# Performance work log

Hardware: AMD Instinct MI355X
Metric: run time of the kernel (lower is better)

## Reference

```python
import jax, jax.numpy as jnp
import numpy as np

B, LT, LS, D, H, F = 4, 1024, 1024, 1024, 16, 4096
HD = D // H
EPS = 1e-6


def rms_norm(x, g):
    return x / jnp.sqrt(jnp.mean(x * x, axis=-1, keepdims=True) + EPS) * g


def mha(q_in, kv_in, wq, wk, wv, wo, bias):
    # q_in: [B,Lq,D], kv_in: [B,Lk,D], bias broadcastable to [B,H,Lq,Lk]
    b, lq, _ = q_in.shape
    lk = kv_in.shape[1]
    q = (q_in @ wq).reshape(b, lq, H, HD).transpose(0, 2, 1, 3)
    k = (kv_in @ wk).reshape(b, lk, H, HD).transpose(0, 2, 1, 3)
    v = (kv_in @ wv).reshape(b, lk, H, HD).transpose(0, 2, 1, 3)
    s = jnp.einsum('bhqd,bhkd->bhqk', q, k) / np.sqrt(HD).astype(np.float32) + bias
    o = jnp.einsum('bhqk,bhkd->bhqd', jax.nn.softmax(s, axis=-1), v)
    o = o.transpose(0, 2, 1, 3).reshape(b, lq, D) @ wo
    return o, k, v


def setup_inputs() -> dict:
    key = jax.random.key(0)
    ks = jax.random.split(key, 16)
    f = lambda k, sh, s: jax.random.normal(k, sh, jnp.float32) * s
    wscale = 1.0 / float(np.sqrt(D))
    causal = jnp.where(jnp.triu(jnp.ones((LT, LT), bool), 1), jnp.float32(-1e9), jnp.float32(0.0))
    return {
        'x': f(ks[0], (B, LT, D), 1.0),
        'memory': f(ks[1], (B, LS, D), 1.0),
        'position_embedding': f(ks[2], (1, H, LT, LS), 0.02),
        'causal_mask': causal,
        'gamma_sa': jnp.ones((D,), jnp.float32),
        'wq_s': f(ks[3], (D, D), wscale), 'wk_s': f(ks[4], (D, D), wscale),
        'wv_s': f(ks[5], (D, D), wscale), 'wo_s': f(ks[6], (D, D), wscale),
        'gamma_ca': jnp.ones((D,), jnp.float32),
        'wq_c': f(ks[7], (D, D), wscale), 'wk_c': f(ks[8], (D, D), wscale),
        'wv_c': f(ks[9], (D, D), wscale), 'wo_c': f(ks[10], (D, D), wscale),
        'gamma_m': jnp.ones((D,), jnp.float32),
        'w1': f(ks[11], (D, F), wscale), 'w2': f(ks[12], (F, D), 1.0 / float(np.sqrt(F))),
    }


def reference(x, memory, position_embedding, causal_mask,
              gamma_sa, wq_s, wk_s, wv_s, wo_s,
              gamma_ca, wq_c, wk_c, wv_c, wo_c,
              gamma_m, w1, w2):
    # self-attention block (pre-RMSNorm, causal mask, residual)
    h = rms_norm(x, gamma_sa)
    a, k_s, v_s = mha(h, h, wq_s, wk_s, wv_s, wo_s, causal_mask[None, None, :, :])
    attn_x = a + x
    # cross-attention block (position-embedding bias on scores, residual)
    h2 = rms_norm(attn_x, gamma_ca)
    c, k_c, v_c = mha(h2, memory, wq_c, wk_c, wv_c, wo_c, position_embedding)
    cross_x = c + attn_x
    # FFN block
    h3 = rms_norm(cross_x, gamma_m)
    mlp_x = jax.nn.relu(h3 @ w1) @ w2 + cross_x
    return mlp_x, (k_s, v_s), (k_c, v_c)
```

## Files before the change

### kernel.cpp

```cpp
#include <hip/hip_runtime.h>
#include <stdint.h>
#include <stddef.h>

typedef __bf16 bf16_t;
typedef __attribute__((ext_vector_type(8))) __bf16 bf16x8;
typedef __attribute__((ext_vector_type(4))) float f32x4;

#define LT 1024
#define LS 1024
#define DM 1024
#define NH 16
#define HD 64
#define FF 4096
#define BB 4

__device__ __forceinline__ void gld_lds16(const bf16_t* g, bf16_t* l) {
    __builtin_amdgcn_global_load_lds(
        (const __attribute__((address_space(1))) void*)g,
        (__attribute__((address_space(3))) void*)l, 16, 0, 0);
}

__global__ __launch_bounds__(256) void transpose_f2bf(
    const float* __restrict__ in, bf16_t* __restrict__ out, int R, int C)
{
    __shared__ float tile[32][33];
    int bx = blockIdx.x * 32;
    int by = blockIdx.y * 32;
    int tx = threadIdx.x, ty = threadIdx.y;
#pragma unroll
    for (int j = 0; j < 4; j++)
        tile[ty + j * 8][tx] = in[(size_t)(by + ty + j * 8) * C + bx + tx];
    __syncthreads();
#pragma unroll
    for (int j = 0; j < 4; j++)
        out[(size_t)(bx + ty + j * 8) * R + by + tx] = (bf16_t)tile[tx][ty + j * 8];
}

__global__ __launch_bounds__(256) void transpose_bf(
    const bf16_t* __restrict__ in, bf16_t* __restrict__ out)
{
    __shared__ bf16_t tile[32][33];
    int bh = blockIdx.z;
    int r0 = blockIdx.x * 32;
    int c0 = blockIdx.y * 32;
    const bf16_t* ib = in + (size_t)bh * LT * HD;
    bf16_t* ob = out + (size_t)bh * HD * LT;
    int tx = threadIdx.x, ty = threadIdx.y;
#pragma unroll
    for (int j = 0; j < 4; j++)
        tile[ty + j * 8][tx] = ib[(size_t)(r0 + ty + j * 8) * HD + c0 + tx];
    __syncthreads();
#pragma unroll
    for (int j = 0; j < 4; j++)
        ob[(size_t)(c0 + ty + j * 8) * LT + r0 + tx] = tile[tx][ty + j * 8];
}

__global__ __launch_bounds__(256) void f2bf_kernel(
    const float* __restrict__ in, bf16_t* __restrict__ out, size_t n)
{
    size_t i = ((size_t)blockIdx.x * 256 + threadIdx.x) * 4;
    if (i + 3 < n) {
        float4 v = *(const float4*)&in[i];
        out[i + 0] = (bf16_t)v.x;
        out[i + 1] = (bf16_t)v.y;
        out[i + 2] = (bf16_t)v.z;
        out[i + 3] = (bf16_t)v.w;
    }
}

__global__ __launch_bounds__(256) void reduce2_res(
    const float* __restrict__ p, const float* __restrict__ res,
    float* __restrict__ out)
{
    const size_t MN = (size_t)BB * LT * DM;
    size_t i = ((size_t)blockIdx.x * 256 + threadIdx.x) * 4;
    float4 a = *(const float4*)&p[i];
    float4 b = *(const float4*)&p[i + MN];
    float4 r = *(const float4*)&res[i];
    float4 o;
    o.x = a.x + b.x + r.x; o.y = a.y + b.y + r.y;
    o.z = a.z + b.z + r.z; o.w = a.w + b.w + r.w;
    *(float4*)&out[i] = o;
}

__global__ __launch_bounds__(256) void rmsnorm_kernel(
    const float* __restrict__ x, const float* __restrict__ g,
    bf16_t* __restrict__ out)
{
    __shared__ float red[4];
    int row = blockIdx.x;
    int t = threadIdx.x;
    int lane = t & 63, w = t >> 6;
    const float* xr = x + (size_t)row * DM;
    float4 v = *(const float4*)&xr[t * 4];
    float ss = v.x * v.x + v.y * v.y + v.z * v.z + v.w * v.w;
#pragma unroll
    for (int off = 32; off > 0; off >>= 1) ss += __shfl_down(ss, off, 64);
    if (lane == 0) red[w] = ss;
    __syncthreads();
    float tot = red[0] + red[1] + red[2] + red[3];
    float inv = rsqrtf(tot * (1.0f / DM) + 1e-6f);
    float4 gv = *(const float4*)&g[t * 4];
    bf16_t* o = out + (size_t)row * DM + t * 4;
    o[0] = (bf16_t)(v.x * inv * gv.x);
    o[1] = (bf16_t)(v.y * inv * gv.y);
    o[2] = (bf16_t)(v.z * inv * gv.z);
    o[3] = (bf16_t)(v.w * inv * gv.w);
}

#define GEMM_BODY(Aptr, Btptr, Kstride, kBeg, kEnd)                              \
    for (int k0 = (kBeg); k0 < (kEnd); k0 += 64) {                               \
        __syncthreads();                                                         \
        _Pragma("unroll")                                                        \
        for (int i = 0; i < 4; i++) {                                            \
            int p = i * 256 + t;                                                 \
            int row = p >> 3;                                                    \
            int g = (p & 7) ^ (row & 7);                                         \
            gld_lds16(&(Aptr)[(size_t)(m0 + row) * (Kstride) + k0 + g * 8],      \
                      &lA[p * 8]);                                               \
            gld_lds16(&(Btptr)[(size_t)(n0 + row) * (Kstride) + k0 + g * 8],     \
                      &lB[p * 8]);                                               \
        }                                                                        \
        __syncthreads();                                                         \
        _Pragma("unroll")                                                        \
        for (int s = 0; s < 2; s++) {                                            \
            bf16x8 af[4], bfr[4];                                                \
            _Pragma("unroll")                                                    \
            for (int mt = 0; mt < 4; mt++) {                                     \
                int r = wr * 64 + mt * 16 + l15;                                 \
                af[mt] = *(const bf16x8*)&lA[((r << 3) + ((s * 4 + quad) ^ (r & 7))) << 3]; \
            }                                                                    \
            _Pragma("unroll")                                                    \
            for (int nt = 0; nt < 4; nt++) {                                     \
                int r = wc * 64 + nt * 16 + l15;                                 \
                bfr[nt] = *(const bf16x8*)&lB[((r << 3) + ((s * 4 + quad) ^ (r & 7))) << 3]; \
            }                                                                    \
            _Pragma("unroll")                                                    \
            for (int mt = 0; mt < 4; mt++)                                       \
                _Pragma("unroll")                                                \
                for (int nt = 0; nt < 4; nt++)                                   \
                    acc[mt][nt] = __builtin_amdgcn_mfma_f32_16x16x32_bf16(       \
                        af[mt], bfr[nt], acc[mt][nt], 0, 0, 0);                  \
        }                                                                        \
    }

__global__ __launch_bounds__(256) void gemm_qkv(
    const bf16_t* __restrict__ A1, const bf16_t* __restrict__ B1, int nb1,
    const bf16_t* __restrict__ A2, const bf16_t* __restrict__ B2, int secbase2,
    bf16_t* __restrict__ qb,
    float* __restrict__ kF, bf16_t* __restrict__ kB,
    float* __restrict__ vF, bf16_t* __restrict__ vB)
{
    __shared__ bf16_t lA[128 * 64];
    __shared__ bf16_t lB[128 * 64];
    const int t = threadIdx.x;
    const int lane = t & 63, w = t >> 6;
    const int quad = lane >> 4, l15 = lane & 15;
    const int m0 = blockIdx.x * 128;
    const int wr = w >> 1, wc = w & 1;

    const bf16_t* A; const bf16_t* Bt; int n0, sec0;
    if ((int)blockIdx.y < nb1) { A = A1; Bt = B1; n0 = blockIdx.y * 128; sec0 = 0; }
    else { A = A2; Bt = B2; n0 = (blockIdx.y - nb1) * 128; sec0 = secbase2; }

    f32x4 acc[4][4] = {};
    GEMM_BODY(A, Bt, 1024, 0, 1024)

#pragma unroll
    for (int mt = 0; mt < 4; mt++) {
#pragma unroll
        for (int nt = 0; nt < 4; nt++) {
#pragma unroll
            for (int r = 0; r < 4; r++) {
                int row = m0 + wr * 64 + mt * 16 + quad * 4 + r;
                int col = n0 + wc * 64 + nt * 16 + l15;
                float v = acc[mt][nt][r];
                int b = row >> 10, tp = row & 1023;
                int sec = sec0 + (col >> 10);
                int c10 = col & 1023;
                int h = c10 >> 6, d = c10 & 63;
                size_t idx = (((size_t)(b * NH + h)) << 16) + (size_t)tp * HD + d;
                if (sec == 0) {
                    qb[idx] = (bf16_t)v;
                } else if (sec == 1) {
                    kF[idx] = v;
                    kB[idx] = (bf16_t)v;
                } else {
                    vF[idx] = v;
                    vB[idx] = (bf16_t)v;
                }
            }
        }
    }
}

#define EP_RES 0
#define EP_RELU 1
#define EP_PART 2

template <int EP, int KSPLIT>
__global__ __launch_bounds__(256) void gemm_bt(
    const bf16_t* __restrict__ A, const bf16_t* __restrict__ Bt,
    int N, int K,
    float* __restrict__ outF, const float* __restrict__ res,
    bf16_t* __restrict__ outB)
{
    __shared__ bf16_t lA[128 * 64];
    __shared__ bf16_t lB[128 * 64];
    const int t = threadIdx.x;
    const int lane = t & 63, w = t >> 6;
    const int quad = lane >> 4, l15 = lane & 15;
    const int m0 = blockIdx.x * 128, n0 = blockIdx.y * 128;
    const int wr = w >> 1, wc = w & 1;
    const int Kc = K / KSPLIT;
    const int kBeg = blockIdx.z * Kc;

    f32x4 acc[4][4] = {};
    GEMM_BODY(A, Bt, K, kBeg, kBeg + Kc)

    float* dst = outF;
    if constexpr (EP == EP_PART)
        dst = outF + (size_t)blockIdx.z * (size_t)gridDim.x * 128 * N;

#pragma unroll
    for (int mt = 0; mt < 4; mt++) {
#pragma unroll
        for (int nt = 0; nt < 4; nt++) {
#pragma unroll
            for (int r = 0; r < 4; r++) {
                int row = m0 + wr * 64 + mt * 16 + quad * 4 + r;
                int col = n0 + wc * 64 + nt * 16 + l15;
                float v = acc[mt][nt][r];
                if constexpr (EP == EP_RES) {
                    dst[(size_t)row * N + col] = v + res[(size_t)row * N + col];
                } else if constexpr (EP == EP_RELU) {
                    outB[(size_t)row * N + col] = (bf16_t)fmaxf(v, 0.0f);
                } else {
                    dst[(size_t)row * N + col] = v;
                }
            }
        }
    }
}

template <bool CAUSAL>
__global__ __launch_bounds__(256) void flash_attn(
    const bf16_t* __restrict__ Q, const bf16_t* __restrict__ Kb,
    const bf16_t* __restrict__ Vt, const float* __restrict__ bias,
    bf16_t* __restrict__ O)
{
    __shared__ bf16_t lK[64 * 64];
    __shared__ bf16_t lV[64 * 64];
    __shared__ bf16_t lP[4][16 * 64];
    const int t = threadIdx.x;
    const int lane = t & 63, w = t >> 6;
    const int quad = lane >> 4, l15 = lane & 15;
    const int qt = blockIdx.x;
    const int bh = blockIdx.y;
    const int b = bh >> 4, h = bh & 15;
    const int q0 = qt * 64;

    const bf16_t* qbase = Q + (size_t)bh * LT * HD;
    const bf16_t* kbase = Kb + (size_t)bh * LS * HD;
    const bf16_t* vbase = Vt + (size_t)bh * HD * LS;

    bf16x8 qf[2];
    int qrow = q0 + w * 16 + l15;
#pragma unroll
    for (int s = 0; s < 2; s++)
        qf[s] = *(const bf16x8*)&qbase[(size_t)qrow * HD + s * 32 + quad * 8];

    f32x4 acc_o[4] = {};
    float m_i[4], l_i[4];
#pragma unroll
    for (int r = 0; r < 4; r++) { m_i[r] = -3.0e38f; l_i[r] = 0.0f; }

    const int nkt = CAUSAL ? (qt + 1) : (LS / 64);
    for (int kt = 0; kt < nkt; kt++) {
        const int kb = kt * 64;
        __syncthreads();
#pragma unroll
        for (int i = 0; i < 2; i++) {
            int p = i * 256 + t;
            int row = p >> 3;
            int g = (p & 7) ^ (row & 7);
            gld_lds16(&kbase[(size_t)(kb + row) * HD + g * 8], &lK[p * 8]);
            gld_lds16(&vbase[(size_t)row * LS + kb + g * 8], &lV[p * 8]);
        }
        __syncthreads();

        f32x4 sacc[4];
#pragma unroll
        for (int nt = 0; nt < 4; nt++) {
            f32x4 sa = {};
#pragma unroll
            for (int s = 0; s < 2; s++) {
                int r = nt * 16 + l15;
                bf16x8 kf = *(const bf16x8*)&lK[((r << 3) + ((s * 4 + quad) ^ (r & 7))) << 3];
                sa = __builtin_amdgcn_mfma_f32_16x16x32_bf16(qf[s], kf, sa, 0, 0, 0);
            }
            sacc[nt] = sa;
        }

        float sval[4][4];
        float tmax[4];
#pragma unroll
        for (int r = 0; r < 4; r++) tmax[r] = -3.0e38f;
#pragma unroll
        for (int nt = 0; nt < 4; nt++) {
            int col = kb + nt * 16 + l15;
#pragma unroll
            for (int r = 0; r < 4; r++) {
                int row = q0 + w * 16 + quad * 4 + r;
                float v = sacc[nt][r] * 0.125f;
                if constexpr (CAUSAL) {
                    if (col > row) v = -1e9f;
                } else {
                    v += bias[((size_t)(h * LT + row)) * LS + col];
                }
                sval[nt][r] = v;
                tmax[r] = fmaxf(tmax[r], v);
            }
        }
#pragma unroll
        for (int r = 0; r < 4; r++) {
            float v = tmax[r];
            v = fmaxf(v, __shfl_xor(v, 1, 64));
            v = fmaxf(v, __shfl_xor(v, 2, 64));
            v = fmaxf(v, __shfl_xor(v, 4, 64));
            v = fmaxf(v, __shfl_xor(v, 8, 64));
            tmax[r] = v;
        }
        float alpha[4], rsum[4];
#pragma unroll
        for (int r = 0; r < 4; r++) {
            float mn = fmaxf(m_i[r], tmax[r]);
            alpha[r] = __expf(m_i[r] - mn);
            m_i[r] = mn;
            rsum[r] = 0.0f;
        }
#pragma unroll
        for (int nt = 0; nt < 4; nt++) {
#pragma unroll
            for (int r = 0; r < 4; r++) {
                float p = __expf(sval[nt][r] - m_i[r]);
                rsum[r] += p;
                int pr = quad * 4 + r;
                int gcol = nt * 2 + (l15 >> 3);
                lP[w][((pr << 3) + (gcol ^ (pr & 7))) * 8 + (l15 & 7)] = (bf16_t)p;
            }
        }
#pragma unroll
        for (int r = 0; r < 4; r++) {
            float v = rsum[r];
            v += __shfl_xor(v, 1, 64);
            v += __shfl_xor(v, 2, 64);
            v += __shfl_xor(v, 4, 64);
            v += __shfl_xor(v, 8, 64);
            l_i[r] = l_i[r] * alpha[r] + v;
        }
#pragma unroll
        for (int dt = 0; dt < 4; dt++)
#pragma unroll
            for (int r = 0; r < 4; r++)
                acc_o[dt][r] *= alpha[r];

#pragma unroll
        for (int s = 0; s < 2; s++) {
            bf16x8 pf = *(const bf16x8*)&lP[w][((l15 << 3) + ((s * 4 + quad) ^ (l15 & 7))) << 3];
#pragma unroll
            for (int dt = 0; dt < 4; dt++) {
                int r = dt * 16 + l15;
                bf16x8 vf = *(const bf16x8*)&lV[((r << 3) + ((s * 4 + quad) ^ (r & 7))) << 3];
                acc_o[dt] = __builtin_amdgcn_mfma_f32_16x16x32_bf16(pf, vf, acc_o[dt], 0, 0, 0);
            }
        }
    }

#pragma unroll
    for (int dt = 0; dt < 4; dt++) {
#pragma unroll
        for (int r = 0; r < 4; r++) {
            int row = q0 + w * 16 + quad * 4 + r;
            int col = h * HD + dt * 16 + l15;
            float v = acc_o[dt][r] / l_i[r];
            O[((size_t)(b * LT + row)) * DM + col] = (bf16_t)v;
        }
    }
}

extern "C" void kernel_launch(void* const* d_in, const int* in_sizes, int n_in,
                              void* d_out, int out_size, void* d_ws, size_t ws_size,
                              hipStream_t stream)
{
    (void)in_sizes; (void)n_in; (void)out_size; (void)ws_size;
    const float* x    = (const float*)d_in[0];
    const float* mem  = (const float*)d_in[1];
    const float* pemb = (const float*)d_in[2];
    const float* g_sa = (const float*)d_in[4];
    const float* wq_s = (const float*)d_in[5];
    const float* wk_s = (const float*)d_in[6];
    const float* wv_s = (const float*)d_in[7];
    const float* wo_s = (const float*)d_in[8];
    const float* g_ca = (const float*)d_in[9];
    const float* wq_c = (const float*)d_in[10];
    const float* wk_c = (const float*)d_in[11];
    const float* wv_c = (const float*)d_in[12];
    const float* wo_c = (const float*)d_in[13];
    const float* g_m  = (const float*)d_in[14];
    const float* w1   = (const float*)d_in[15];
    const float* w2   = (const float*)d_in[16];
    float* out = (float*)d_out;

    const size_t OFF_KS = 4u * 1024 * 1024;
    const size_t OFF_VS = 8u * 1024 * 1024;
    const size_t OFF_KC = 12u * 1024 * 1024;
    const size_t OFF_VC = 16u * 1024 * 1024;

    char* ws = (char*)d_ws;
    const size_t MB = 1024 * 1024;
    bf16_t* wqkvTs = (bf16_t*)(ws + 0 * MB);
    bf16_t* woTs   = (bf16_t*)(ws + 6 * MB);
    bf16_t* wqTc   = (bf16_t*)(ws + 8 * MB);
    bf16_t* wkvTc  = (bf16_t*)(ws + 10 * MB);
    bf16_t* woTc   = (bf16_t*)(ws + 14 * MB);
    bf16_t* w1T    = (bf16_t*)(ws + 16 * MB);
    bf16_t* w2T    = (bf16_t*)(ws + 24 * MB);
    bf16_t* membf  = (bf16_t*)(ws + 32 * MB);
    bf16_t* hbuf   = (bf16_t*)(ws + 40 * MB);
    bf16_t* qbuf   = (bf16_t*)(ws + 48 * MB);
    bf16_t* kbuf   = (bf16_t*)(ws + 56 * MB);
    bf16_t* vbuf   = (bf16_t*)(ws + 64 * MB);
    bf16_t* vTbuf  = (bf16_t*)(ws + 72 * MB);
    bf16_t* Obuf   = (bf16_t*)(ws + 80 * MB);
    float*  attn_x  = (float*)(ws + 88 * MB);
    float*  cross_x = (float*)(ws + 112 * MB);
    bf16_t* ffnmid  = (bf16_t*)(ws + 48 * MB);
    float*  part    = (float*)(ws + 80 * MB);

    dim3 tb(32, 8);
    transpose_f2bf<<<dim3(32, 32), tb, 0, stream>>>(wq_s, wqkvTs, DM, DM);
    transpose_f2bf<<<dim3(32, 32), tb, 0, stream>>>(wk_s, wqkvTs + 1024 * 1024, DM, DM);
    transpose_f2bf<<<dim3(32, 32), tb, 0, stream>>>(wv_s, wqkvTs + 2 * 1024 * 1024, DM, DM);
    transpose_f2bf<<<dim3(32, 32), tb, 0, stream>>>(wo_s, woTs, DM, DM);
    transpose_f2bf<<<dim3(32, 32), tb, 0, stream>>>(wq_c, wqTc, DM, DM);
    transpose_f2bf<<<dim3(32, 32), tb, 0, stream>>>(wk_c, wkvTc, DM, DM);
    transpose_f2bf<<<dim3(32, 32), tb, 0, stream>>>(wv_c, wkvTc + 1024 * 1024, DM, DM);
    transpose_f2bf<<<dim3(32, 32), tb, 0, stream>>>(wo_c, woTc, DM, DM);
    transpose_f2bf<<<dim3(128, 32), tb, 0, stream>>>(w1, w1T, DM, FF);
    transpose_f2bf<<<dim3(32, 128), tb, 0, stream>>>(w2, w2T, FF, DM);

    f2bf_kernel<<<4096, 256, 0, stream>>>(mem, membf, (size_t)BB * LS * DM);

    rmsnorm_kernel<<<BB * LT, 256, 0, stream>>>(x, g_sa, hbuf);
    gemm_qkv<<<dim3(32, 24), 256, 0, stream>>>(
        hbuf, wqkvTs, 24, hbuf, wqkvTs, 0,
        qbuf, out + OFF_KS, kbuf, out + OFF_VS, vbuf);
    transpose_bf<<<dim3(32, 2, 64), tb, 0, stream>>>(vbuf, vTbuf);
    flash_attn<true><<<dim3(16, 64), 256, 0, stream>>>(qbuf, kbuf, vTbuf, nullptr, Obuf);
    gemm_bt<EP_RES, 1><<<dim3(32, 8), 256, 0, stream>>>(
        Obuf, woTs, 1024, 1024, attn_x, x, nullptr);

    rmsnorm_kernel<<<BB * LT, 256, 0, stream>>>(attn_x, g_ca, hbuf);
    gemm_qkv<<<dim3(32, 24), 256, 0, stream>>>(
        hbuf, wqTc, 8, membf, wkvTc, 1,
        qbuf, out + OFF_KC, kbuf, out + OFF_VC, vbuf);
    transpose_bf<<<dim3(32, 2, 64), tb, 0, stream>>>(vbuf, vTbuf);
    flash_attn<false><<<dim3(16, 64), 256, 0, stream>>>(qbuf, kbuf, vTbuf, pemb, Obuf);
    gemm_bt<EP_RES, 1><<<dim3(32, 8), 256, 0, stream>>>(
        Obuf, woTc, 1024, 1024, cross_x, attn_x, nullptr);

    rmsnorm_kernel<<<BB * LT, 256, 0, stream>>>(cross_x, g_m, hbuf);
    gemm_bt<EP_RELU, 1><<<dim3(32, 32), 256, 0, stream>>>(
        hbuf, w1T, 4096, 1024, nullptr, nullptr, ffnmid);
    gemm_bt<EP_PART, 2><<<dim3(32, 8, 2), 256, 0, stream>>>(
        ffnmid, w2T, 1024, 4096, part, nullptr, nullptr);
    reduce2_res<<<4096, 256, 0, stream>>>(part, cross_x, out);
}
```

Before: 658.0 us.

## Double-buffer K/V tiles and prefetch bias in flash attention; batch weight transposes

The flash attention kernel now double-buffers K and V tiles in LDS and prefetches the next tile, plus the next tile's position bias values into registers, while computing the current one. Explicit vmcnt waits and barriers replace the two __syncthreads per iteration. Block ordering is remapped so blocks sharing a head's bias run adjacently, and launch bounds request 4 blocks per CU. Eight separate weight-transpose launches are merged into one batched launch, which cuts launch overhead but adds LDS use and register pressure in attention.

```diff
diff --git a/kernel.cpp b/kernel.cpp
--- a/kernel.cpp
+++ b/kernel.cpp
@@ -34,6 +34,24 @@
 #pragma unroll
     for (int j = 0; j < 4; j++)
         out[(size_t)(bx + ty + j * 8) * R + by + tx] = (bf16_t)tile[tx][ty + j * 8];
+}
+
+struct TPtrs { const float* in[8]; bf16_t* out[8]; };
+__global__ __launch_bounds__(256) void transpose8_f2bf(TPtrs p)
+{
+    __shared__ float tile[32][33];
+    const float* in = p.in[blockIdx.z];
+    bf16_t* out = p.out[blockIdx.z];
+    int bx = blockIdx.x * 32;
+    int by = blockIdx.y * 32;
+    int tx = threadIdx.x, ty = threadIdx.y;
+#pragma unroll
+    for (int j = 0; j < 4; j++)
+        tile[ty + j * 8][tx] = in[(size_t)(by + ty + j * 8) * 1024 + bx + tx];
+    __syncthreads();
+#pragma unroll
+    for (int j = 0; j < 4; j++)
+        out[(size_t)(bx + ty + j * 8) * 1024 + by + tx] = (bf16_t)tile[tx][ty + j * 8];
 }
 
 __global__ __launch_bounds__(256) void transpose_bf(
@@ -244,25 +262,27 @@
 }
 
 template <bool CAUSAL>
-__global__ __launch_bounds__(256) void flash_attn(
+__global__ __launch_bounds__(256, 4) void flash_attn(
     const bf16_t* __restrict__ Q, const bf16_t* __restrict__ Kb,
     const bf16_t* __restrict__ Vt, const float* __restrict__ bias,
     bf16_t* __restrict__ O)
 {
-    __shared__ bf16_t lK[64 * 64];
-    __shared__ bf16_t lV[64 * 64];
+    __shared__ bf16_t lK[2][64 * 64];
+    __shared__ bf16_t lV[2][64 * 64];
     __shared__ bf16_t lP[4][16 * 64];
     const int t = threadIdx.x;
     const int lane = t & 63, w = t >> 6;
     const int quad = lane >> 4, l15 = lane & 15;
     const int qt = blockIdx.x;
-    const int bh = blockIdx.y;
-    const int b = bh >> 4, h = bh & 15;
+    const int yy = blockIdx.y;
+    const int h = yy >> 2, b = yy & 3;
+    const int bhd = b * NH + h;
     const int q0 = qt * 64;
 
-    const bf16_t* qbase = Q + (size_t)bh * LT * HD;
-    const bf16_t* kbase = Kb + (size_t)bh * LS * HD;
-    const bf16_t* vbase = Vt + (size_t)bh * HD * LS;
+    const bf16_t* qbase = Q + (size_t)bhd * LT * HD;
+    const bf16_t* kbase = Kb + (size_t)bhd * LS * HD;
+    const bf16_t* vbase = Vt + (size_t)bhd * HD * LS;
+    const float* bbase = bias + (size_t)h * LT * LS;
 
     bf16x8 qf[2];
     int qrow = q0 + w * 16 + l15;
@@ -276,19 +296,61 @@
     for (int r = 0; r < 4; r++) { m_i[r] = -3.0e38f; l_i[r] = 0.0f; }
 
     const int nkt = CAUSAL ? (qt + 1) : (LS / 64);
+
+#pragma unroll
+    for (int i = 0; i < 2; i++) {
+        int p = i * 256 + t;
+        int row = p >> 3;
+        int g = (p & 7) ^ (row & 7);
+        gld_lds16(&kbase[(size_t)row * HD + g * 8], &lK[0][p * 8]);
+        gld_lds16(&vbase[(size_t)row * LS + g * 8], &lV[0][p * 8]);
+    }
+    float bnxt[16], bcur[16];
+    if constexpr (!CAUSAL) {
+#pragma unroll
+        for (int nt = 0; nt < 4; nt++)
+#pragma unroll
+            for (int r = 0; r < 4; r++)
+                bnxt[nt * 4 + r] =
+                    bbase[(size_t)(q0 + w * 16 + quad * 4 + r) * LS + nt * 16 + l15];
+    }
+
     for (int kt = 0; kt < nkt; kt++) {
+        const int d = kt & 1;
+        const int nxt = kt + 1;
+        if constexpr (!CAUSAL) {
+#pragma unroll
+            for (int i = 0; i < 16; i++) bcur[i] = bnxt[i];
+        }
+        if (nxt < nkt) {
+            const int nb = nxt * 64;
+            const int nd = nxt & 1;
+#pragma unroll
+            for (int i = 0; i < 2; i++) {
+                int p = i * 256 + t;
+                int row = p >> 3;
+                int g = (p & 7) ^ (row & 7);
+                gld_lds16(&kbase[(size_t)(nb + row) * HD + g * 8], &lK[nd][p * 8]);
+                gld_lds16(&vbase[(size_t)row * LS + nb + g * 8], &lV[nd][p * 8]);
+            }
+            if constexpr (!CAUSAL) {
+#pragma unroll
+                for (int nt = 0; nt < 4; nt++)
+#pragma unroll
+                    for (int r = 0; r < 4; r++)
+                        bnxt[nt * 4 + r] =
+                            bbase[(size_t)(q0 + w * 16 + quad * 4 + r) * LS + nb + nt * 16 + l15];
+                asm volatile("s_waitcnt vmcnt(20)" ::: "memory");
+            } else {
+                asm volatile("s_waitcnt vmcnt(4)" ::: "memory");
+            }
+        } else {
+            asm volatile("s_waitcnt vmcnt(0)" ::: "memory");
+        }
+        __builtin_amdgcn_s_barrier();
+        __builtin_amdgcn_sched_barrier(0);
+
         const int kb = kt * 64;
-        __syncthreads();
-#pragma unroll
-        for (int i = 0; i < 2; i++) {
-            int p = i * 256 + t;
-            int row = p >> 3;
-            int g = (p & 7) ^ (row & 7);
-            gld_lds16(&kbase[(size_t)(kb + row) * HD + g * 8], &lK[p * 8]);
-            gld_lds16(&vbase[(size_t)row * LS + kb + g * 8], &lV[p * 8]);
-        }
-        __syncthreads();
-
         f32x4 sacc[4];
 #pragma unroll
         for (int nt = 0; nt < 4; nt++) {
@@ -296,7 +358,7 @@
 #pragma unroll
             for (int s = 0; s < 2; s++) {
                 int r = nt * 16 + l15;
-                bf16x8 kf = *(const bf16x8*)&lK[((r << 3) + ((s * 4 + quad) ^ (r & 7))) << 3];
+                bf16x8 kf = *(const bf16x8*)&lK[d][((r << 3) + ((s * 4 + quad) ^ (r & 7))) << 3];
                 sa = __builtin_amdgcn_mfma_f32_16x16x32_bf16(qf[s], kf, sa, 0, 0, 0);
             }
             sacc[nt] = sa;
@@ -316,7 +378,7 @@
                 if constexpr (CAUSAL) {
                     if (col > row) v = -1e9f;
                 } else {
-                    v += bias[((size_t)(h * LT + row)) * LS + col];
+                    v += bcur[nt * 4 + r];
                 }
                 sval[nt][r] = v;
                 tmax[r] = fmaxf(tmax[r], v);
@@ -371,10 +433,11 @@
 #pragma unroll
             for (int dt = 0; dt < 4; dt++) {
                 int r = dt * 16 + l15;
-                bf16x8 vf = *(const bf16x8*)&lV[((r << 3) + ((s * 4 + quad) ^ (r & 7))) << 3];
+                bf16x8 vf = *(const bf16x8*)&lV[d][((r << 3) + ((s * 4 + quad) ^ (r & 7))) << 3];
                 acc_o[dt] = __builtin_amdgcn_mfma_f32_16x16x32_bf16(pf, vf, acc_o[dt], 0, 0, 0);
             }
         }
+        __builtin_amdgcn_s_barrier();
     }
 
 #pragma unroll
@@ -439,14 +502,16 @@
     float*  part    = (float*)(ws + 80 * MB);
 
     dim3 tb(32, 8);
-    transpose_f2bf<<<dim3(32, 32), tb, 0, stream>>>(wq_s, wqkvTs, DM, DM);
-    transpose_f2bf<<<dim3(32, 32), tb, 0, stream>>>(wk_s, wqkvTs + 1024 * 1024, DM, DM);
-    transpose_f2bf<<<dim3(32, 32), tb, 0, stream>>>(wv_s, wqkvTs + 2 * 1024 * 1024, DM, DM);
-    transpose_f2bf<<<dim3(32, 32), tb, 0, stream>>>(wo_s, woTs, DM, DM);
-    transpose_f2bf<<<dim3(32, 32), tb, 0, stream>>>(wq_c, wqTc, DM, DM);
-    transpose_f2bf<<<dim3(32, 32), tb, 0, stream>>>(wk_c, wkvTc, DM, DM);
-    transpose_f2bf<<<dim3(32, 32), tb, 0, stream>>>(wv_c, wkvTc + 1024 * 1024, DM, DM);
-    transpose_f2bf<<<dim3(32, 32), tb, 0, stream>>>(wo_c, woTc, DM, DM);
+    TPtrs tp;
+    tp.in[0] = wq_s; tp.out[0] = wqkvTs;
+    tp.in[1] = wk_s; tp.out[1] = wqkvTs + 1024 * 1024;
+    tp.in[2] = wv_s; tp.out[2] = wqkvTs + 2 * 1024 * 1024;
+    tp.in[3] = wo_s; tp.out[3] = woTs;
+    tp.in[4] = wq_c; tp.out[4] = wqTc;
+    tp.in[5] = wk_c; tp.out[5] = wkvTc;
+    tp.in[6] = wv_c; tp.out[6] = wkvTc + 1024 * 1024;
+    tp.in[7] = wo_c; tp.out[7] = woTc;
+    transpose8_f2bf<<<dim3(32, 32, 8), tb, 0, stream>>>(tp);
     transpose_f2bf<<<dim3(128, 32), tb, 0, stream>>>(w1, w1T, DM, FF);
     transpose_f2bf<<<dim3(32, 128), tb, 0, stream>>>(w2, w2T, FF, DM);
 
```

Result: faster. 618.7 us (-6.0%).
